# Kernel tuning notes

Hardware: AMD Instinct MI355X
Metric: run time of the kernel (lower is better)

The kernel has to match this reference:

```python
import jax, jax.numpy as jnp
import numpy as np

N = 4096   # support size
B = 512    # number of histograms (columns)


def setup_inputs() -> dict:
    key = jax.random.key(0)
    kU, kP, kK = jax.random.split(key, 3)
    # u must satisfy u < lamda; uniform [0,1) with lamda=10 is safe.
    U = jax.random.uniform(kU, (N, B), dtype=jnp.float32)
    # strictly positive histograms (avoid log(0))
    P = jax.random.uniform(kP, (N, B), dtype=jnp.float32) + 0.01
    # positive Gibbs kernel
    K = jax.random.uniform(kK, (N, N), dtype=jnp.float32) + 1e-3
    return {"U": U, "P": P, "K": K, "eps": 1, "lamda": 10}


def reference(U, P, K, eps, lamda):
    """Vectorized OTModel.OT_unbal: sum over columns of the primal unbalanced OT
    value reconstructed from dual potential U.  gamma_ij = a_i * K_ij * f_j is
    never materialized; all reductions over gamma are contracted analytically.
    """
    eps = jnp.float32(eps)
    lamda = jnp.float32(lamda)
    # f in log domain: (lamda/eps) * log(lamda/(lamda-u))          [N, B]
    flog = (lamda / eps) * jnp.log(lamda / (lamda - U))
    f = jnp.exp(flog)
    # alpha/eps with the mean-scale stabilization from get_alpha_unbal
    scale = flog.mean(axis=0)                                      # [B]
    KF_stab = K @ jnp.exp(flog - scale)                            # [N, B]
    alpha_over_eps = jnp.log(P) - (jnp.log(KF_stab) + scale)       # [N, B]
    a = jnp.exp(alpha_over_eps)                                    # exp(alpha/eps)
    Kf = K @ f                                                     # [N, B]
    # (gamma @ flog).sum() = sum_i a_i * (K @ (f * flog))_i
    term1 = jnp.sum(a * (K @ (f * flog)))
    # (gamma.T @ (alpha/eps)).sum() = sum_i a_i * (alpha/eps)_i * (K @ f)_i
    term2 = jnp.sum(a * alpha_over_eps * Kf)
    # gamma.sum()
    term3 = jnp.sum(a * Kf)
    # gamma.sum(0)_j = f_j * (K^T @ a)_j
    gcol = f * (K.T @ a)                                           # [N, B]
    # q from get_q_unbal (unstabilized, as in the original)
    q = (lamda / (lamda - U)) ** (lamda / eps + 1.0) * (K.T @ (P / Kf))
    # KL(a,b) = sum(a*log(a/b) - a)   (inputs strictly positive here)
    kl = jnp.sum(gcol * jnp.log(gcol / q) - gcol)
    return eps * (term1 + term2 - term3) + lamda * kl
```

## Files before the change

### kernel.cpp

```cpp
#include <hip/hip_runtime.h>

#define NN 4096
#define BB 512

typedef __attribute__((ext_vector_type(4))) float f32x4;
typedef __attribute__((ext_vector_type(2))) long long2v;
typedef unsigned short ushort;
typedef unsigned char uchar;
typedef unsigned int uint;
typedef __attribute__((ext_vector_type(4))) ushort ushort4v;

#define ASCALE 16384.0f
#define AINV   6.103515625e-05f

__device__ __forceinline__ float scal_val(const void* p) {
    int b = *(const int*)p;
    if (b >= 1 && b <= 1000000) return (float)b;
    return __int_as_float(b);
}

__device__ __forceinline__ ushort f2bf(float x) {
    unsigned u = __float_as_uint(x);
    u += 0x7fffu + ((u >> 16) & 1u);
    return (ushort)(u >> 16);
}
__device__ __forceinline__ float bf2f(ushort b) {
    return __uint_as_float((uint)b << 16);
}

__device__ __forceinline__ uint pack4_fp8(float a, float b, float c, float d) {
    int v = __builtin_amdgcn_cvt_pk_fp8_f32(a, b, 0, false);
    v = __builtin_amdgcn_cvt_pk_fp8_f32(c, d, v, true);
    return (uint)v;
}

__device__ __forceinline__ void gload16(const void* g, void* l) {
    __builtin_amdgcn_global_load_lds(
        (const __attribute__((address_space(1))) unsigned int*)g,
        (__attribute__((address_space(3))) unsigned int*)l, 16, 0, 0);
}

__device__ __forceinline__ double wave_sum(double v) {
#pragma unroll
    for (int s = 32; s > 0; s >>= 1) v += __shfl_down(v, s, 64);
    return v;
}

__device__ __forceinline__ int kperm(int kk) {
    int c = kk >> 3;
    return (c & 3) * 16 + (c >> 2) * 8 + (kk & 7);
}
__device__ __forceinline__ int bpos(int row, int pp) {
    return (((pp >> 4) ^ ((row >> 1) & 3)) << 4) | (pp & 15);
}



__global__ __launch_bounds__(256) void k_prep(const float* __restrict__ K,
                                              const float* __restrict__ U,
                                              uchar* __restrict__ Kb,
                                              uchar* __restrict__ KTb,
                                              uchar* __restrict__ fT,
                                              const void* epsp, const void* lamp) {
    __shared__ float tile[64][65];
    const int t = threadIdx.x;
    const int tx = t & 15, ty = t >> 4;
    const int bid = blockIdx.x;
    const int pp = kperm(tx * 4);

    if (bid < 4096) {
        const int c0 = (bid & 63) * 64, r0 = (bid >> 6) * 64;
#pragma unroll
        for (int it = 0; it < 4; ++it) {
            int row = ty + it * 16;
            float4 v = *(const float4*)&K[(size_t)(r0 + row) * NN + c0 + tx * 4];
            int i = r0 + row;
            int off = (((i >> 7) * 64 + (c0 >> 6)) << 13) + (i & 127) * 64 +
                      bpos(row, pp);
            *(uint*)&Kb[off] = pack4_fp8(v.x, v.y, v.z, v.w);
            tile[row][tx * 4 + 0] = v.x;
            tile[row][tx * 4 + 1] = v.y;
            tile[row][tx * 4 + 2] = v.z;
            tile[row][tx * 4 + 3] = v.w;
        }
        __syncthreads();
#pragma unroll
        for (int it = 0; it < 4; ++it) {
            int row = ty + it * 16;
            int i = c0 + row;
            int off = (((i >> 7) * 64 + (r0 >> 6)) << 13) + (i & 127) * 64 +
                      bpos(row, pp);
            *(uint*)&KTb[off] =
                pack4_fp8(tile[tx * 4 + 0][row], tile[tx * 4 + 1][row],
                          tile[tx * 4 + 2][row], tile[tx * 4 + 3][row]);
        }
    } else {
        const int r = bid - 4096;
        const int c0 = (r & 7) * 64;
        const int r0 = (r >> 3) * 64;
        const float eps = scal_val(epsp), lam = scal_val(lamp);
        const float rr = lam / eps;
#pragma unroll
        for (int it = 0; it < 4; ++it) {
            int row = ty + it * 16;
            float4 v = *(const float4*)&U[(size_t)(r0 + row) * BB + c0 + tx * 4];
            float uu[4] = {v.x, v.y, v.z, v.w};
#pragma unroll
            for (int k = 0; k < 4; ++k) {
                float L = __logf(lam / (lam - uu[k]));
                tile[row][tx * 4 + k] = __expf(rr * L);
            }
        }
        __syncthreads();
#pragma unroll
        for (int it = 0; it < 4; ++it) {
            int row = ty + it * 16;
            int j = c0 + row;
            int off = (((j >> 6) * 64 + (r0 >> 6)) << 12) + (j & 63) * 64 +
                      bpos(row, pp);
            *(uint*)&fT[off] =
                pack4_fp8(tile[tx * 4 + 0][row], tile[tx * 4 + 1][row],
                          tile[tx * 4 + 2][row], tile[tx * 4 + 3][row]);
        }
    }
}

__global__ __launch_bounds__(256) void k_gemm1(const uchar* __restrict__ Kb,
                                               const uchar* __restrict__ fT,
                                               ushort* __restrict__ Y1b) {
    __shared__ __align__(16) uchar As[2][128 * 64];
    __shared__ __align__(16) uchar Bf[2][64 * 64];

    const int tid = threadIdx.x;
    const int lane = tid & 63;
    const int w = tid >> 6;
    const int wm = w & 1, wn = w >> 1;
    const int bid = blockIdx.x;
    const int kh = bid & 3;
    const int i0 = ((bid >> 2) & 31) * 128;
    const int j0 = (bid >> 7) * 64;
    const int quad = lane >> 4;
    const int l15 = lane & 15;
    const int sw = (l15 >> 1) & 3;

    f32x4 zero = {0.f, 0.f, 0.f, 0.f};
    f32x4 acc[4][2];
#pragma unroll
    for (int mt = 0; mt < 4; ++mt)
#pragma unroll
        for (int nt = 0; nt < 2; ++nt) acc[mt][nt] = zero;

    const uchar* apanel = Kb + ((size_t)(i0 >> 7) << 19);
    const uchar* bpanel = fT + ((size_t)(j0 >> 6) << 18);

    auto stage = [&](int ks, int b) {
        const uchar* ga = apanel + ((size_t)ks << 13) + w * 2048 + lane * 16;
        gload16(ga, &As[b][w * 2048]);
        gload16(ga + 1024, &As[b][w * 2048 + 1024]);
        const uchar* gb = bpanel + ((size_t)ks << 12) + w * 1024 + lane * 16;
        gload16(gb, &Bf[b][w * 1024]);
    };

    const int ks0 = kh * 16;
    stage(ks0, 0);
    __syncthreads();
    const int uoff = ((quad ^ sw) << 4);
    for (int step = 0; step < 16; ++step) {
        const int cur = step & 1;
        if (step < 15) stage(ks0 + step + 1, cur ^ 1);
        long2v av[4], bv[2];
#pragma unroll
        for (int mt = 0; mt < 4; ++mt)
            av[mt] = *(const long2v*)&As[cur][(wm * 64 + mt * 16 + l15) * 64 + uoff];
#pragma unroll
        for (int nt = 0; nt < 2; ++nt)
            bv[nt] = *(const long2v*)&Bf[cur][(wn * 32 + nt * 16 + l15) * 64 + uoff];
#pragma unroll
        for (int mt = 0; mt < 4; ++mt)
#pragma unroll
            for (int nt = 0; nt < 2; ++nt) {
                acc[mt][nt] = __builtin_amdgcn_mfma_f32_16x16x32_fp8_fp8(
                    av[mt].x, bv[nt].x, acc[mt][nt], 0, 0, 0);
                acc[mt][nt] = __builtin_amdgcn_mfma_f32_16x16x32_fp8_fp8(
                    av[mt].y, bv[nt].y, acc[mt][nt], 0, 0, 0);
            }
        __syncthreads();
    }

    ushort* o1 = Y1b + (size_t)kh * NN * BB;
#pragma unroll
    for (int mt = 0; mt < 4; ++mt)
#pragma unroll
        for (int nt = 0; nt < 2; ++nt) {
            const int ib = i0 + wm * 64 + mt * 16 + quad * 4;
            const int j = j0 + wn * 32 + nt * 16 + l15;
#pragma unroll
            for (int r = 0; r < 4; ++r)
                o1[(size_t)(ib + r) * BB + j] = f2bf(acc[mt][nt][r]);
        }
}

__global__ __launch_bounds__(256) void k_epi(const ushort* __restrict__ Y1b,
                                             const float* __restrict__ P,
                                             uchar* __restrict__ aT,
                                             double* __restrict__ parts) {
    __shared__ float ta[64][65];
    __shared__ double bred[4][2];
    const int t = threadIdx.x;
    const int lane = t & 63;
    const int w = t >> 6;
    const int tx = t & 15, ty = t >> 4;
    const int j0 = blockIdx.x * 64;
    const int i0 = blockIdx.y * 64;
    const int bid = blockIdx.y * 8 + blockIdx.x;
    const size_t H = (size_t)NN * BB;
    const int pp = kperm(tx * 4);

    double t2 = 0.0, t3 = 0.0;
#pragma unroll
    for (int it = 0; it < 4; ++it) {
        int row = ty + it * 16;
        size_t off = (size_t)(i0 + row) * BB + j0 + tx * 4;
        ushort4v q0 = *(const ushort4v*)(Y1b + off);
        ushort4v q1 = *(const ushort4v*)(Y1b + H + off);
        ushort4v q2 = *(const ushort4v*)(Y1b + 2 * H + off);
        ushort4v q3 = *(const ushort4v*)(Y1b + 3 * H + off);
        float4 p4 = *(const float4*)(P + off);
        float pv[4] = {p4.x, p4.y, p4.z, p4.w};
#pragma unroll
        for (int e = 0; e < 4; ++e) {
            float y1 = bf2f(q0[e]) + bf2f(q1[e]) + bf2f(q2[e]) + bf2f(q3[e]);
            float aij = pv[e] / y1;
            t2 += (double)(pv[e] * __logf(aij));
            t3 += (double)pv[e];
            ta[row][tx * 4 + e] = aij * ASCALE;
        }
    }
    __syncthreads();
#pragma unroll
    for (int it = 0; it < 4; ++it) {
        int row = ty + it * 16;
        int j = j0 + row;
        int off = (((j >> 6) * 64 + (i0 >> 6)) << 12) + (j & 63) * 64 +
                  bpos(row, pp);
        *(uint*)&aT[off] =
            pack4_fp8(ta[tx * 4 + 0][row], ta[tx * 4 + 1][row],
                      ta[tx * 4 + 2][row], ta[tx * 4 + 3][row]);
    }

    t2 = wave_sum(t2); t3 = wave_sum(t3);
    if (lane == 0) { bred[w][0] = t2; bred[w][1] = t3; }
    __syncthreads();
    if (t == 0) {
        double b = 0, c = 0;
#pragma unroll
        for (int ww = 0; ww < 4; ++ww) { b += bred[ww][0]; c += bred[ww][1]; }
        parts[2048 + bid] = b;
        parts[2560 + bid] = c;
    }
}

__global__ __launch_bounds__(256) void k_gemm2(const uchar* __restrict__ KTb,
                                               const uchar* __restrict__ aT,
                                               const float* __restrict__ U,
                                               const void* epsp, const void* lamp,
                                               double* __restrict__ parts) {
    __shared__ __align__(16) uchar As[2][128 * 64];
    __shared__ __align__(16) uchar Bs[2][64 * 64];
    __shared__ double bred[4][2];

    const float eps = scal_val(epsp), lam = scal_val(lamp);
    const float rr = lam / eps;
    const int tid = threadIdx.x;
    const int lane = tid & 63;
    const int w = tid >> 6;
    const int wm = w & 1, wn = w >> 1;
    const int bid = blockIdx.x;
    const int kh = bid & 3;
    const int i0 = ((bid >> 2) & 31) * 128;
    const int j0 = (bid >> 7) * 64;
    const int quad = lane >> 4;
    const int l15 = lane & 15;
    const int sw = (l15 >> 1) & 3;

    f32x4 zero = {0.f, 0.f, 0.f, 0.f};
    f32x4 acc[4][2];
#pragma unroll
    for (int mt = 0; mt < 4; ++mt)
#pragma unroll
        for (int nt = 0; nt < 2; ++nt) acc[mt][nt] = zero;

    const uchar* apanel = KTb + ((size_t)(i0 >> 7) << 19);
    const uchar* bpanel = aT + ((size_t)(j0 >> 6) << 18);

    auto stage = [&](int ks, int b) {
        const uchar* ga = apanel + ((size_t)ks << 13) + w * 2048 + lane * 16;
        gload16(ga, &As[b][w * 2048]);
        gload16(ga + 1024, &As[b][w * 2048 + 1024]);
        const uchar* gb = bpanel + ((size_t)ks << 12) + w * 1024 + lane * 16;
        gload16(gb, &Bs[b][w * 1024]);
    };

    const int ks0 = kh * 16;
    stage(ks0, 0);
    __syncthreads();
    const int uoff = ((quad ^ sw) << 4);
    for (int step = 0; step < 16; ++step) {
        const int cur = step & 1;
        if (step < 15) stage(ks0 + step + 1, cur ^ 1);
        long2v av[4], bv[2];
#pragma unroll
        for (int mt = 0; mt < 4; ++mt)
            av[mt] = *(const long2v*)&As[cur][(wm * 64 + mt * 16 + l15) * 64 + uoff];
#pragma unroll
        for (int nt = 0; nt < 2; ++nt)
            bv[nt] = *(const long2v*)&Bs[cur][(wn * 32 + nt * 16 + l15) * 64 + uoff];
#pragma unroll
        for (int mt = 0; mt < 4; ++mt)
#pragma unroll
            for (int nt = 0; nt < 2; ++nt) {
                acc[mt][nt] = __builtin_amdgcn_mfma_f32_16x16x32_fp8_fp8(
                    av[mt].x, bv[nt].x, acc[mt][nt], 0, 0, 0);
                acc[mt][nt] = __builtin_amdgcn_mfma_f32_16x16x32_fp8_fp8(
                    av[mt].y, bv[nt].y, acc[mt][nt], 0, 0, 0);
            }
        __syncthreads();
    }

    double t1p = 0.0, klp = 0.0;
#pragma unroll
    for (int mt = 0; mt < 4; ++mt)
#pragma unroll
        for (int nt = 0; nt < 2; ++nt) {
            const int ib = i0 + wm * 64 + mt * 16 + quad * 4;
            const int j = j0 + wn * 32 + nt * 16 + l15;
#pragma unroll
            for (int r = 0; r < 4; ++r) {
                float s = acc[mt][nt][r] * AINV;
                float u = U[(size_t)(ib + r) * BB + j];
                float L = __logf(lam / (lam - u));
                float fv = __expf(rr * L);
                t1p += (double)(fv * rr * L * s);
                klp -= (double)(fv * (1.0f + L) * s);
            }
        }

    t1p = wave_sum(t1p); klp = wave_sum(klp);
    if (lane == 0) { bred[w][0] = t1p; bred[w][1] = klp; }
    __syncthreads();
    if (tid == 0) {
        double a = 0, b = 0;
#pragma unroll
        for (int ww = 0; ww < 4; ++ww) { a += bred[ww][0]; b += bred[ww][1]; }
        parts[bid] = a;
        parts[1024 + bid] = b;
    }
}

__global__ __launch_bounds__(256) void k_final(const double* __restrict__ parts,
                                               const void* epsp, const void* lamp,
                                               float* __restrict__ out) {
    __shared__ double red[4][4];
    const int tid = threadIdx.x;
    const int lane = tid & 63, w = tid >> 6;
    double s0 = 0.0, s1 = 0.0, s2 = 0.0, s3 = 0.0;
    for (int i = tid; i < 1024; i += 256) {
        s0 += parts[i];
        s1 += parts[1024 + i];
    }
    for (int i = tid; i < 512; i += 256) {
        s2 += parts[2048 + i];
        s3 += parts[2560 + i];
    }
    s0 = wave_sum(s0); s1 = wave_sum(s1); s2 = wave_sum(s2); s3 = wave_sum(s3);
    if (lane == 0) { red[w][0] = s0; red[w][1] = s1; red[w][2] = s2; red[w][3] = s3; }
    __syncthreads();
    if (tid == 0) {
        double t1 = 0, kl = 0, t2 = 0, t3 = 0;
#pragma unroll
        for (int ww = 0; ww < 4; ++ww) {
            t1 += red[ww][0]; kl += red[ww][1]; t2 += red[ww][2]; t3 += red[ww][3];
        }
        float eps = scal_val(epsp), lam = scal_val(lamp);
        out[0] = (float)((double)eps * (t1 + t2 - t3) + (double)lam * kl);
    }
}

extern "C" void kernel_launch(void* const* d_in, const int* in_sizes, int n_in,
                              void* d_out, int out_size, void* d_ws, size_t ws_size,
                              hipStream_t stream) {
    const float* U = (const float*)d_in[0];
    const float* P = (const float*)d_in[1];
    const float* K = (const float*)d_in[2];
    const void* epsp = d_in[3];
    const void* lamp = d_in[4];

    double* parts = (double*)d_ws;
    char* base = (char*)d_ws + (64 << 10);
    uchar* Kb   = (uchar*)base;
    uchar* KTb  = (uchar*)(base + ((size_t)16 << 20));
    uchar* fT   = (uchar*)(base + ((size_t)32 << 20));
    uchar* aT   = (uchar*)(base + ((size_t)34 << 20));
    ushort* Y1b = (ushort*)(base + ((size_t)36 << 20));

    k_prep<<<4608, 256, 0, stream>>>(K, U, Kb, KTb, fT, epsp, lamp);
    k_gemm1<<<1024, 256, 0, stream>>>(Kb, fT, Y1b);
    k_epi<<<dim3(8, 64), 256, 0, stream>>>(Y1b, P, aT, parts);
    k_gemm2<<<1024, 256, 0, stream>>>(KTb, aT, U, epsp, lamp, parts);
    k_final<<<1, 256, 0, stream>>>(parts, epsp, lamp, (float*)d_out);
}
```

Before: 164.6 us.

## Switch FP8 GEMMs to 16x16x128 scaled MFMA with 128-wide K tiles

Both GEMMs now use the gfx950 scaled MFMA 16x16x128 f8f6f4 instruction with unit scales in place of pairs of 16x16x32 fp8 MFMAs. The packed fp8 layouts for K, K^T, f and a are rewritten into 128-byte K rows with an XOR swizzle, and the LDS tiles double in size. Split-K drops from 4 to 2, which halves the grid to 512 blocks, and the partial sums are stored as fp32 instead of bf16 so the epilogue reads two slabs instead of four. The change cuts the MFMA instruction count and split-K reduction traffic, at the cost of fewer blocks in flight and more LDS per block, which may lower occupancy.

```diff
diff --git a/kernel.cpp b/kernel.cpp
--- a/kernel.cpp
+++ b/kernel.cpp
@@ -4,14 +4,15 @@
 #define BB 512
 
 typedef __attribute__((ext_vector_type(4))) float f32x4;
-typedef __attribute__((ext_vector_type(2))) long long2v;
+typedef __attribute__((ext_vector_type(4))) int i32x4;
+typedef __attribute__((ext_vector_type(8))) int i32x8;
 typedef unsigned short ushort;
 typedef unsigned char uchar;
 typedef unsigned int uint;
-typedef __attribute__((ext_vector_type(4))) ushort ushort4v;
 
 #define ASCALE 16384.0f
 #define AINV   6.103515625e-05f
+#define SCL1   0x7f7f7f7f
 
 __device__ __forceinline__ float scal_val(const void* p) {
     int b = *(const int*)p;
@@ -19,15 +20,6 @@
     return __int_as_float(b);
 }
 
-__device__ __forceinline__ ushort f2bf(float x) {
-    unsigned u = __float_as_uint(x);
-    u += 0x7fffu + ((u >> 16) & 1u);
-    return (ushort)(u >> 16);
-}
-__device__ __forceinline__ float bf2f(ushort b) {
-    return __uint_as_float((uint)b << 16);
-}
-
 __device__ __forceinline__ uint pack4_fp8(float a, float b, float c, float d) {
     int v = __builtin_amdgcn_cvt_pk_fp8_f32(a, b, 0, false);
     v = __builtin_amdgcn_cvt_pk_fp8_f32(c, d, v, true);
@@ -46,14 +38,23 @@
     return v;
 }
 
-__device__ __forceinline__ int kperm(int kk) {
-    int c = kk >> 3;
-    return (c & 3) * 16 + (c >> 2) * 8 + (kk & 7);
-}
-__device__ __forceinline__ int bpos(int row, int pp) {
-    return (((pp >> 4) ^ ((row >> 1) & 3)) << 4) | (pp & 15);
-}
-
+__device__ __forceinline__ int offA(int i, int k) {
+    return (((i >> 7) * 32 + (k >> 7)) << 14) + ((i & 127) << 7) +
+           ((((k >> 4) & 7) ^ (i & 7)) << 4) + (k & 15);
+}
+__device__ __forceinline__ int offB(int j, int k) {
+    return (((j >> 6) * 32 + (k >> 7)) << 13) + ((j & 63) << 7) +
+           ((((k >> 4) & 7) ^ (j & 7)) << 4) + (k & 15);
+}
+
+__device__ __forceinline__ i32x8 frag128(const uchar* rowbase, int u0byte) {
+    i32x4 lo = *(const i32x4*)(rowbase + u0byte);
+    i32x4 hi = *(const i32x4*)(rowbase + (u0byte ^ 16));
+    i32x8 r;
+    r[0] = lo[0]; r[1] = lo[1]; r[2] = lo[2]; r[3] = lo[3];
+    r[4] = hi[0]; r[5] = hi[1]; r[6] = hi[2]; r[7] = hi[3];
+    return r;
+}
 
 
 __global__ __launch_bounds__(256) void k_prep(const float* __restrict__ K,
@@ -66,18 +67,15 @@
     const int t = threadIdx.x;
     const int tx = t & 15, ty = t >> 4;
     const int bid = blockIdx.x;
-    const int pp = kperm(tx * 4);
 
     if (bid < 4096) {
         const int c0 = (bid & 63) * 64, r0 = (bid >> 6) * 64;
 #pragma unroll
         for (int it = 0; it < 4; ++it) {
             int row = ty + it * 16;
-            float4 v = *(const float4*)&K[(size_t)(r0 + row) * NN + c0 + tx * 4];
             int i = r0 + row;
-            int off = (((i >> 7) * 64 + (c0 >> 6)) << 13) + (i & 127) * 64 +
-                      bpos(row, pp);
-            *(uint*)&Kb[off] = pack4_fp8(v.x, v.y, v.z, v.w);
+            float4 v = *(const float4*)&K[(size_t)i * NN + c0 + tx * 4];
+            *(uint*)&Kb[offA(i, c0 + tx * 4)] = pack4_fp8(v.x, v.y, v.z, v.w);
             tile[row][tx * 4 + 0] = v.x;
             tile[row][tx * 4 + 1] = v.y;
             tile[row][tx * 4 + 2] = v.z;
@@ -88,9 +86,8 @@
         for (int it = 0; it < 4; ++it) {
             int row = ty + it * 16;
             int i = c0 + row;
-            int off = (((i >> 7) * 64 + (r0 >> 6)) << 13) + (i & 127) * 64 +
-                      bpos(row, pp);
-            *(uint*)&KTb[off] =
+            int k = r0 + tx * 4;
+            *(uint*)&KTb[offA(i, k)] =
                 pack4_fp8(tile[tx * 4 + 0][row], tile[tx * 4 + 1][row],
                           tile[tx * 4 + 2][row], tile[tx * 4 + 3][row]);
         }
@@ -116,9 +113,8 @@
         for (int it = 0; it < 4; ++it) {
             int row = ty + it * 16;
             int j = c0 + row;
-            int off = (((j >> 6) * 64 + (r0 >> 6)) << 12) + (j & 63) * 64 +
-                      bpos(row, pp);
-            *(uint*)&fT[off] =
+            int k = r0 + tx * 4;
+            *(uint*)&fT[offB(j, k)] =
                 pack4_fp8(tile[tx * 4 + 0][row], tile[tx * 4 + 1][row],
                           tile[tx * 4 + 2][row], tile[tx * 4 + 3][row]);
         }
@@ -127,21 +123,21 @@
 
 __global__ __launch_bounds__(256) void k_gemm1(const uchar* __restrict__ Kb,
                                                const uchar* __restrict__ fT,
-                                               ushort* __restrict__ Y1b) {
-    __shared__ __align__(16) uchar As[2][128 * 64];
-    __shared__ __align__(16) uchar Bf[2][64 * 64];
+                                               float* __restrict__ Y1f) {
+    __shared__ __align__(16) uchar As[2][128 * 128];
+    __shared__ __align__(16) uchar Bf[2][64 * 128];
 
     const int tid = threadIdx.x;
     const int lane = tid & 63;
     const int w = tid >> 6;
     const int wm = w & 1, wn = w >> 1;
     const int bid = blockIdx.x;
-    const int kh = bid & 3;
-    const int i0 = ((bid >> 2) & 31) * 128;
-    const int j0 = (bid >> 7) * 64;
+    const int kh = bid & 1;
+    const int i0 = ((bid >> 1) & 31) * 128;
+    const int j0 = (bid >> 6) * 64;
     const int quad = lane >> 4;
     const int l15 = lane & 15;
-    const int sw = (l15 >> 1) & 3;
+    const int u0b = (((quad << 1) ^ (l15 & 7)) << 4);
 
     f32x4 zero = {0.f, 0.f, 0.f, 0.f};
     f32x4 acc[4][2];
@@ -154,40 +150,39 @@
     const uchar* bpanel = fT + ((size_t)(j0 >> 6) << 18);
 
     auto stage = [&](int ks, int b) {
-        const uchar* ga = apanel + ((size_t)ks << 13) + w * 2048 + lane * 16;
-        gload16(ga, &As[b][w * 2048]);
-        gload16(ga + 1024, &As[b][w * 2048 + 1024]);
-        const uchar* gb = bpanel + ((size_t)ks << 12) + w * 1024 + lane * 16;
-        gload16(gb, &Bf[b][w * 1024]);
+        const uchar* ga = apanel + ((size_t)ks << 14) + w * 4096 + lane * 16;
+        gload16(ga, &As[b][w * 4096]);
+        gload16(ga + 1024, &As[b][w * 4096 + 1024]);
+        gload16(ga + 2048, &As[b][w * 4096 + 2048]);
+        gload16(ga + 3072, &As[b][w * 4096 + 3072]);
+        const uchar* gb = bpanel + ((size_t)ks << 13) + w * 2048 + lane * 16;
+        gload16(gb, &Bf[b][w * 2048]);
+        gload16(gb + 1024, &Bf[b][w * 2048 + 1024]);
     };
 
     const int ks0 = kh * 16;
     stage(ks0, 0);
     __syncthreads();
-    const int uoff = ((quad ^ sw) << 4);
     for (int step = 0; step < 16; ++step) {
         const int cur = step & 1;
         if (step < 15) stage(ks0 + step + 1, cur ^ 1);
-        long2v av[4], bv[2];
+        i32x8 av[4], bv[2];
 #pragma unroll
         for (int mt = 0; mt < 4; ++mt)
-            av[mt] = *(const long2v*)&As[cur][(wm * 64 + mt * 16 + l15) * 64 + uoff];
+            av[mt] = frag128(&As[cur][(wm * 64 + mt * 16 + l15) << 7], u0b);
 #pragma unroll
         for (int nt = 0; nt < 2; ++nt)
-            bv[nt] = *(const long2v*)&Bf[cur][(wn * 32 + nt * 16 + l15) * 64 + uoff];
+            bv[nt] = frag128(&Bf[cur][(wn * 32 + nt * 16 + l15) << 7], u0b);
 #pragma unroll
         for (int mt = 0; mt < 4; ++mt)
 #pragma unroll
-            for (int nt = 0; nt < 2; ++nt) {
-                acc[mt][nt] = __builtin_amdgcn_mfma_f32_16x16x32_fp8_fp8(
-                    av[mt].x, bv[nt].x, acc[mt][nt], 0, 0, 0);
-                acc[mt][nt] = __builtin_amdgcn_mfma_f32_16x16x32_fp8_fp8(
-                    av[mt].y, bv[nt].y, acc[mt][nt], 0, 0, 0);
-            }
+            for (int nt = 0; nt < 2; ++nt)
+                acc[mt][nt] = __builtin_amdgcn_mfma_scale_f32_16x16x128_f8f6f4(
+                    av[mt], bv[nt], acc[mt][nt], 0, 0, 0, SCL1, 0, SCL1);
         __syncthreads();
     }
 
-    ushort* o1 = Y1b + (size_t)kh * NN * BB;
+    float* o1 = Y1f + (size_t)kh * NN * BB;
 #pragma unroll
     for (int mt = 0; mt < 4; ++mt)
 #pragma unroll
@@ -196,11 +191,11 @@
             const int j = j0 + wn * 32 + nt * 16 + l15;
 #pragma unroll
             for (int r = 0; r < 4; ++r)
-                o1[(size_t)(ib + r) * BB + j] = f2bf(acc[mt][nt][r]);
-        }
-}
-
-__global__ __launch_bounds__(256) void k_epi(const ushort* __restrict__ Y1b,
+                o1[(size_t)(ib + r) * BB + j] = acc[mt][nt][r];
+        }
+}
+
+__global__ __launch_bounds__(256) void k_epi(const float* __restrict__ Y1f,
                                              const float* __restrict__ P,
                                              uchar* __restrict__ aT,
                                              double* __restrict__ parts) {
@@ -214,25 +209,21 @@
     const int i0 = blockIdx.y * 64;
     const int bid = blockIdx.y * 8 + blockIdx.x;
     const size_t H = (size_t)NN * BB;
-    const int pp = kperm(tx * 4);
 
     double t2 = 0.0, t3 = 0.0;
 #pragma unroll
     for (int it = 0; it < 4; ++it) {
         int row = ty + it * 16;
         size_t off = (size_t)(i0 + row) * BB + j0 + tx * 4;
-        ushort4v q0 = *(const ushort4v*)(Y1b + off);
-        ushort4v q1 = *(const ushort4v*)(Y1b + H + off);
-        ushort4v q2 = *(const ushort4v*)(Y1b + 2 * H + off);
-        ushort4v q3 = *(const ushort4v*)(Y1b + 3 * H + off);
-        float4 p4 = *(const float4*)(P + off);
-        float pv[4] = {p4.x, p4.y, p4.z, p4.w};
+        f32x4 q0 = *(const f32x4*)(Y1f + off);
+        f32x4 q1 = *(const f32x4*)(Y1f + H + off);
+        f32x4 p4 = *(const f32x4*)(P + off);
 #pragma unroll
         for (int e = 0; e < 4; ++e) {
-            float y1 = bf2f(q0[e]) + bf2f(q1[e]) + bf2f(q2[e]) + bf2f(q3[e]);
-            float aij = pv[e] / y1;
-            t2 += (double)(pv[e] * __logf(aij));
-            t3 += (double)pv[e];
+            float y1 = q0[e] + q1[e];
+            float aij = p4[e] / y1;
+            t2 += (double)(p4[e] * __logf(aij));
+            t3 += (double)p4[e];
             ta[row][tx * 4 + e] = aij * ASCALE;
         }
     }
@@ -241,9 +232,7 @@
     for (int it = 0; it < 4; ++it) {
         int row = ty + it * 16;
         int j = j0 + row;
-        int off = (((j >> 6) * 64 + (i0 >> 6)) << 12) + (j & 63) * 64 +
-                  bpos(row, pp);
-        *(uint*)&aT[off] =
+        *(uint*)&aT[offB(j, i0 + tx * 4)] =
             pack4_fp8(ta[tx * 4 + 0][row], ta[tx * 4 + 1][row],
                       ta[tx * 4 + 2][row], ta[tx * 4 + 3][row]);
     }
@@ -265,8 +254,8 @@
                                                const float* __restrict__ U,
                                                const void* epsp, const void* lamp,
                                                double* __restrict__ parts) {
-    __shared__ __align__(16) uchar As[2][128 * 64];
-    __shared__ __align__(16) uchar Bs[2][64 * 64];
+    __shared__ __align__(16) uchar As[2][128 * 128];
+    __shared__ __align__(16) uchar Bs[2][64 * 128];
     __shared__ double bred[4][2];
 
     const float eps = scal_val(epsp), lam = scal_val(lamp);
@@ -276,12 +265,12 @@
     const int w = tid >> 6;
     const int wm = w & 1, wn = w >> 1;
     const int bid = blockIdx.x;
-    const int kh = bid & 3;
-    const int i0 = ((bid >> 2) & 31) * 128;
-    const int j0 = (bid >> 7) * 64;
+    const int kh = bid & 1;
+    const int i0 = ((bid >> 1) & 31) * 128;
+    const int j0 = (bid >> 6) * 64;
     const int quad = lane >> 4;
     const int l15 = lane & 15;
-    const int sw = (l15 >> 1) & 3;
+    const int u0b = (((quad << 1) ^ (l15 & 7)) << 4);
 
     f32x4 zero = {0.f, 0.f, 0.f, 0.f};
     f32x4 acc[4][2];
@@ -294,36 +283,35 @@
     const uchar* bpanel = aT + ((size_t)(j0 >> 6) << 18);
 
     auto stage = [&](int ks, int b) {
-        const uchar* ga = apanel + ((size_t)ks << 13) + w * 2048 + lane * 16;
-        gload16(ga, &As[b][w * 2048]);
-        gload16(ga + 1024, &As[b][w * 2048 + 1024]);
-        const uchar* gb = bpanel + ((size_t)ks << 12) + w * 1024 + lane * 16;
-        gload16(gb, &Bs[b][w * 1024]);
+        const uchar* ga = apanel + ((size_t)ks << 14) + w * 4096 + lane * 16;
+        gload16(ga, &As[b][w * 4096]);
+        gload16(ga + 1024, &As[b][w * 4096 + 1024]);
+        gload16(ga + 2048, &As[b][w * 4096 + 2048]);
+        gload16(ga + 3072, &As[b][w * 4096 + 3072]);
+        const uchar* gb = bpanel + ((size_t)ks << 13) + w * 2048 + lane * 16;
+        gload16(gb, &Bs[b][w * 2048]);
+        gload16(gb + 1024, &Bs[b][w * 2048 + 1024]);
     };
 
     const int ks0 = kh * 16;
     stage(ks0, 0);
     __syncthreads();
-    const int uoff = ((quad ^ sw) << 4);
     for (int step = 0; step < 16; ++step) {
         const int cur = step & 1;
         if (step < 15) stage(ks0 + step + 1, cur ^ 1);
-        long2v av[4], bv[2];
+        i32x8 av[4], bv[2];
 #pragma unroll
         for (int mt = 0; mt < 4; ++mt)
-            av[mt] = *(const long2v*)&As[cur][(wm * 64 + mt * 16 + l15) * 64 + uoff];
+            av[mt] = frag128(&As[cur][(wm * 64 + mt * 16 + l15) << 7], u0b);
 #pragma unroll
         for (int nt = 0; nt < 2; ++nt)
-            bv[nt] = *(const long2v*)&Bs[cur][(wn * 32 + nt * 16 + l15) * 64 + uoff];
+            bv[nt] = frag128(&Bs[cur][(wn * 32 + nt * 16 + l15) << 7], u0b);
 #pragma unroll
         for (int mt = 0; mt < 4; ++mt)
 #pragma unroll
-            for (int nt = 0; nt < 2; ++nt) {
-                acc[mt][nt] = __builtin_amdgcn_mfma_f32_16x16x32_fp8_fp8(
-                    av[mt].x, bv[nt].x, acc[mt][nt], 0, 0, 0);
-                acc[mt][nt] = __builtin_amdgcn_mfma_f32_16x16x32_fp8_fp8(
-                    av[mt].y, bv[nt].y, acc[mt][nt], 0, 0, 0);
-            }
+            for (int nt = 0; nt < 2; ++nt)
+                acc[mt][nt] = __builtin_amdgcn_mfma_scale_f32_16x16x128_f8f6f4(
+                    av[mt], bv[nt], acc[mt][nt], 0, 0, 0, SCL1, 0, SCL1);
         __syncthreads();
     }
 
@@ -364,11 +352,9 @@
     const int tid = threadIdx.x;
     const int lane = tid & 63, w = tid >> 6;
     double s0 = 0.0, s1 = 0.0, s2 = 0.0, s3 = 0.0;
-    for (int i = tid; i < 1024; i += 256) {
+    for (int i = tid; i < 512; i += 256) {
         s0 += parts[i];
         s1 += parts[1024 + i];
-    }
-    for (int i = tid; i < 512; i += 256) {
         s2 += parts[2048 + i];
         s3 += parts[2560 + i];
     }
@@ -401,11 +387,11 @@
     uchar* KTb  = (uchar*)(base + ((size_t)16 << 20));
     uchar* fT   = (uchar*)(base + ((size_t)32 << 20));
     uchar* aT   = (uchar*)(base + ((size_t)34 << 20));
-    ushort* Y1b = (ushort*)(base + ((size_t)36 << 20));
+    float* Y1f  = (float*)(base + ((size_t)36 << 20));
 
     k_prep<<<4608, 256, 0, stream>>>(K, U, Kb, KTb, fT, epsp, lamp);
-    k_gemm1<<<1024, 256, 0, stream>>>(Kb, fT, Y1b);
-    k_epi<<<dim3(8, 64), 256, 0, stream>>>(Y1b, P, aT, parts);
-    k_gemm2<<<1024, 256, 0, stream>>>(KTb, aT, U, epsp, lamp, parts);
+    k_gemm1<<<512, 256, 0, stream>>>(Kb, fT, Y1f);
+    k_epi<<<dim3(8, 64), 256, 0, stream>>>(Y1f, P, aT, parts);
+    k_gemm2<<<512, 256, 0, stream>>>(KTb, aT, U, epsp, lamp, parts);
     k_final<<<1, 256, 0, stream>>>(parts, epsp, lamp, (float*)d_out);
 }
```

After: 167.9 us. Within noise of the previous version (+2.0%).

## Switch FP8 GEMMs to 32x32x64 scaled MFMA with a new swizzled layout

Applied to the files above, without the earlier changes.

Both FP8 GEMM kernels now issue the MI355X scaled MFMA (32x32x64 f8f6f4, unit scales) instead of many 16x16x32 fp8 MFMAs. Each wave owns a 32-row strip and the full 64 columns, so it makes two large MFMAs per k-step and fewer LDS fragment reads. The prep and epilogue kernels write K, K^T, f^T and a^T with a new swizzle that matches the 64-byte fragments. The wave-to-tile mapping changes, so B fragments are read by every wave and the epilogue store and reduction indexing change too.

```diff
diff --git a/kernel.cpp b/kernel.cpp
--- a/kernel.cpp
+++ b/kernel.cpp
@@ -4,7 +4,9 @@
 #define BB 512
 
 typedef __attribute__((ext_vector_type(4))) float f32x4;
-typedef __attribute__((ext_vector_type(2))) long long2v;
+typedef __attribute__((ext_vector_type(16))) float f32x16;
+typedef __attribute__((ext_vector_type(4))) int i32x4;
+typedef __attribute__((ext_vector_type(8))) int i32x8;
 typedef unsigned short ushort;
 typedef unsigned char uchar;
 typedef unsigned int uint;
@@ -12,6 +14,7 @@
 
 #define ASCALE 16384.0f
 #define AINV   6.103515625e-05f
+#define SCL1   0x7f7f7f7f
 
 __device__ __forceinline__ float scal_val(const void* p) {
     int b = *(const int*)p;
@@ -46,14 +49,23 @@
     return v;
 }
 
-__device__ __forceinline__ int kperm(int kk) {
-    int c = kk >> 3;
-    return (c & 3) * 16 + (c >> 2) * 8 + (kk & 7);
-}
-__device__ __forceinline__ int bpos(int row, int pp) {
-    return (((pp >> 4) ^ ((row >> 1) & 3)) << 4) | (pp & 15);
-}
-
+__device__ __forceinline__ int offA(int i, int k) {
+    return (((i >> 7) * 64 + (k >> 6)) << 13) + ((i & 127) << 6) +
+           ((((k >> 4) & 3) ^ ((i >> 1) & 3)) << 4) + (k & 15);
+}
+__device__ __forceinline__ int offB(int j, int k) {
+    return (((j >> 6) * 64 + (k >> 6)) << 12) + ((j & 63) << 6) +
+           ((((k >> 4) & 3) ^ ((j >> 1) & 3)) << 4) + (k & 15);
+}
+
+__device__ __forceinline__ i32x8 frag64(const uchar* rowbase, int u0byte) {
+    i32x4 lo = *(const i32x4*)(rowbase + u0byte);
+    i32x4 hi = *(const i32x4*)(rowbase + (u0byte ^ 16));
+    i32x8 r;
+    r[0] = lo[0]; r[1] = lo[1]; r[2] = lo[2]; r[3] = lo[3];
+    r[4] = hi[0]; r[5] = hi[1]; r[6] = hi[2]; r[7] = hi[3];
+    return r;
+}
 
 
 __global__ __launch_bounds__(256) void k_prep(const float* __restrict__ K,
@@ -66,18 +78,15 @@
     const int t = threadIdx.x;
     const int tx = t & 15, ty = t >> 4;
     const int bid = blockIdx.x;
-    const int pp = kperm(tx * 4);
 
     if (bid < 4096) {
         const int c0 = (bid & 63) * 64, r0 = (bid >> 6) * 64;
 #pragma unroll
         for (int it = 0; it < 4; ++it) {
             int row = ty + it * 16;
-            float4 v = *(const float4*)&K[(size_t)(r0 + row) * NN + c0 + tx * 4];
             int i = r0 + row;
-            int off = (((i >> 7) * 64 + (c0 >> 6)) << 13) + (i & 127) * 64 +
-                      bpos(row, pp);
-            *(uint*)&Kb[off] = pack4_fp8(v.x, v.y, v.z, v.w);
+            float4 v = *(const float4*)&K[(size_t)i * NN + c0 + tx * 4];
+            *(uint*)&Kb[offA(i, c0 + tx * 4)] = pack4_fp8(v.x, v.y, v.z, v.w);
             tile[row][tx * 4 + 0] = v.x;
             tile[row][tx * 4 + 1] = v.y;
             tile[row][tx * 4 + 2] = v.z;
@@ -88,9 +97,8 @@
         for (int it = 0; it < 4; ++it) {
             int row = ty + it * 16;
             int i = c0 + row;
-            int off = (((i >> 7) * 64 + (r0 >> 6)) << 13) + (i & 127) * 64 +
-                      bpos(row, pp);
-            *(uint*)&KTb[off] =
+            int k = r0 + tx * 4;
+            *(uint*)&KTb[offA(i, k)] =
                 pack4_fp8(tile[tx * 4 + 0][row], tile[tx * 4 + 1][row],
                           tile[tx * 4 + 2][row], tile[tx * 4 + 3][row]);
         }
@@ -116,9 +124,8 @@
         for (int it = 0; it < 4; ++it) {
             int row = ty + it * 16;
             int j = c0 + row;
-            int off = (((j >> 6) * 64 + (r0 >> 6)) << 12) + (j & 63) * 64 +
-                      bpos(row, pp);
-            *(uint*)&fT[off] =
+            int k = r0 + tx * 4;
+            *(uint*)&fT[offB(j, k)] =
                 pack4_fp8(tile[tx * 4 + 0][row], tile[tx * 4 + 1][row],
                           tile[tx * 4 + 2][row], tile[tx * 4 + 3][row]);
         }
@@ -134,21 +141,15 @@
     const int tid = threadIdx.x;
     const int lane = tid & 63;
     const int w = tid >> 6;
-    const int wm = w & 1, wn = w >> 1;
     const int bid = blockIdx.x;
     const int kh = bid & 3;
     const int i0 = ((bid >> 2) & 31) * 128;
     const int j0 = (bid >> 7) * 64;
-    const int quad = lane >> 4;
-    const int l15 = lane & 15;
-    const int sw = (l15 >> 1) & 3;
-
-    f32x4 zero = {0.f, 0.f, 0.f, 0.f};
-    f32x4 acc[4][2];
-#pragma unroll
-    for (int mt = 0; mt < 4; ++mt)
-#pragma unroll
-        for (int nt = 0; nt < 2; ++nt) acc[mt][nt] = zero;
+    const int h = lane >> 5;
+    const int r = lane & 31;
+    const int u0b = (((h << 1) ^ ((r >> 1) & 3)) << 4);
+
+    f32x16 acc0 = {}, acc1 = {};
 
     const uchar* apanel = Kb + ((size_t)(i0 >> 7) << 19);
     const uchar* bpanel = fT + ((size_t)(j0 >> 6) << 18);
@@ -164,40 +165,26 @@
     const int ks0 = kh * 16;
     stage(ks0, 0);
     __syncthreads();
-    const int uoff = ((quad ^ sw) << 4);
     for (int step = 0; step < 16; ++step) {
         const int cur = step & 1;
         if (step < 15) stage(ks0 + step + 1, cur ^ 1);
-        long2v av[4], bv[2];
-#pragma unroll
-        for (int mt = 0; mt < 4; ++mt)
-            av[mt] = *(const long2v*)&As[cur][(wm * 64 + mt * 16 + l15) * 64 + uoff];
-#pragma unroll
-        for (int nt = 0; nt < 2; ++nt)
-            bv[nt] = *(const long2v*)&Bf[cur][(wn * 32 + nt * 16 + l15) * 64 + uoff];
-#pragma unroll
-        for (int mt = 0; mt < 4; ++mt)
-#pragma unroll
-            for (int nt = 0; nt < 2; ++nt) {
-                acc[mt][nt] = __builtin_amdgcn_mfma_f32_16x16x32_fp8_fp8(
-                    av[mt].x, bv[nt].x, acc[mt][nt], 0, 0, 0);
-                acc[mt][nt] = __builtin_amdgcn_mfma_f32_16x16x32_fp8_fp8(
-                    av[mt].y, bv[nt].y, acc[mt][nt], 0, 0, 0);
-            }
+        i32x8 av = frag64(&As[cur][(w * 32 + r) << 6], u0b);
+        i32x8 bv0 = frag64(&Bf[cur][r << 6], u0b);
+        i32x8 bv1 = frag64(&Bf[cur][(32 + r) << 6], u0b);
+        acc0 = __builtin_amdgcn_mfma_scale_f32_32x32x64_f8f6f4(
+            av, bv0, acc0, 0, 0, 0, SCL1, 0, SCL1);
+        acc1 = __builtin_amdgcn_mfma_scale_f32_32x32x64_f8f6f4(
+            av, bv1, acc1, 0, 0, 0, SCL1, 0, SCL1);
         __syncthreads();
     }
 
     ushort* o1 = Y1b + (size_t)kh * NN * BB;
 #pragma unroll
-    for (int mt = 0; mt < 4; ++mt)
-#pragma unroll
-        for (int nt = 0; nt < 2; ++nt) {
-            const int ib = i0 + wm * 64 + mt * 16 + quad * 4;
-            const int j = j0 + wn * 32 + nt * 16 + l15;
-#pragma unroll
-            for (int r = 0; r < 4; ++r)
-                o1[(size_t)(ib + r) * BB + j] = f2bf(acc[mt][nt][r]);
-        }
+    for (int reg = 0; reg < 16; ++reg) {
+        const int row = i0 + w * 32 + (reg & 3) + 8 * (reg >> 2) + 4 * h;
+        o1[(size_t)row * BB + j0 + r] = f2bf(acc0[reg]);
+        o1[(size_t)row * BB + j0 + 32 + r] = f2bf(acc1[reg]);
+    }
 }
 
 __global__ __launch_bounds__(256) void k_epi(const ushort* __restrict__ Y1b,
@@ -214,7 +201,6 @@
     const int i0 = blockIdx.y * 64;
     const int bid = blockIdx.y * 8 + blockIdx.x;
     const size_t H = (size_t)NN * BB;
-    const int pp = kperm(tx * 4);
 
     double t2 = 0.0, t3 = 0.0;
 #pragma unroll
@@ -241,9 +227,7 @@
     for (int it = 0; it < 4; ++it) {
         int row = ty + it * 16;
         int j = j0 + row;
-        int off = (((j >> 6) * 64 + (i0 >> 6)) << 12) + (j & 63) * 64 +
-                  bpos(row, pp);
-        *(uint*)&aT[off] =
+        *(uint*)&aT[offB(j, i0 + tx * 4)] =
             pack4_fp8(ta[tx * 4 + 0][row], ta[tx * 4 + 1][row],
                       ta[tx * 4 + 2][row], ta[tx * 4 + 3][row]);
     }
@@ -274,21 +258,15 @@
     const int tid = threadIdx.x;
     const int lane = tid & 63;
     const int w = tid >> 6;
-    const int wm = w & 1, wn = w >> 1;
     const int bid = blockIdx.x;
     const int kh = bid & 3;
     const int i0 = ((bid >> 2) & 31) * 128;
     const int j0 = (bid >> 7) * 64;
-    const int quad = lane >> 4;
-    const int l15 = lane & 15;
-    const int sw = (l15 >> 1) & 3;
-
-    f32x4 zero = {0.f, 0.f, 0.f, 0.f};
-    f32x4 acc[4][2];
-#pragma unroll
-    for (int mt = 0; mt < 4; ++mt)
-#pragma unroll
-        for (int nt = 0; nt < 2; ++nt) acc[mt][nt] = zero;
+    const int h = lane >> 5;
+    const int r = lane & 31;
+    const int u0b = (((h << 1) ^ ((r >> 1) & 3)) << 4);
+
+    f32x16 acc0 = {}, acc1 = {};
 
     const uchar* apanel = KTb + ((size_t)(i0 >> 7) << 19);
     const uchar* bpanel = aT + ((size_t)(j0 >> 6) << 18);
@@ -304,46 +282,34 @@
     const int ks0 = kh * 16;
     stage(ks0, 0);
     __syncthreads();
-    const int uoff = ((quad ^ sw) << 4);
     for (int step = 0; step < 16; ++step) {
         const int cur = step & 1;
         if (step < 15) stage(ks0 + step + 1, cur ^ 1);
-        long2v av[4], bv[2];
-#pragma unroll
-        for (int mt = 0; mt < 4; ++mt)
-            av[mt] = *(const long2v*)&As[cur][(wm * 64 + mt * 16 + l15) * 64 + uoff];
-#pragma unroll
-        for (int nt = 0; nt < 2; ++nt)
-            bv[nt] = *(const long2v*)&Bs[cur][(wn * 32 + nt * 16 + l15) * 64 + uoff];
-#pragma unroll
-        for (int mt = 0; mt < 4; ++mt)
-#pragma unroll
-            for (int nt = 0; nt < 2; ++nt) {
-                acc[mt][nt] = __builtin_amdgcn_mfma_f32_16x16x32_fp8_fp8(
-                    av[mt].x, bv[nt].x, acc[mt][nt], 0, 0, 0);
-                acc[mt][nt] = __builtin_amdgcn_mfma_f32_16x16x32_fp8_fp8(
-                    av[mt].y, bv[nt].y, acc[mt][nt], 0, 0, 0);
-            }
+        i32x8 av = frag64(&As[cur][(w * 32 + r) << 6], u0b);
+        i32x8 bv0 = frag64(&Bs[cur][r << 6], u0b);
+        i32x8 bv1 = frag64(&Bs[cur][(32 + r) << 6], u0b);
+        acc0 = __builtin_amdgcn_mfma_scale_f32_32x32x64_f8f6f4(
+            av, bv0, acc0, 0, 0, 0, SCL1, 0, SCL1);
+        acc1 = __builtin_amdgcn_mfma_scale_f32_32x32x64_f8f6f4(
+            av, bv1, acc1, 0, 0, 0, SCL1, 0, SCL1);
         __syncthreads();
     }
 
     double t1p = 0.0, klp = 0.0;
 #pragma unroll
-    for (int mt = 0; mt < 4; ++mt)
+    for (int reg = 0; reg < 16; ++reg) {
+        const int ib = i0 + w * 32 + (reg & 3) + 8 * (reg >> 2) + 4 * h;
 #pragma unroll
         for (int nt = 0; nt < 2; ++nt) {
-            const int ib = i0 + wm * 64 + mt * 16 + quad * 4;
-            const int j = j0 + wn * 32 + nt * 16 + l15;
-#pragma unroll
-            for (int r = 0; r < 4; ++r) {
-                float s = acc[mt][nt][r] * AINV;
-                float u = U[(size_t)(ib + r) * BB + j];
-                float L = __logf(lam / (lam - u));
-                float fv = __expf(rr * L);
-                t1p += (double)(fv * rr * L * s);
-                klp -= (double)(fv * (1.0f + L) * s);
-            }
-        }
+            const int j = j0 + nt * 32 + r;
+            float s = (nt ? acc1[reg] : acc0[reg]) * AINV;
+            float u = U[(size_t)ib * BB + j];
+            float L = __logf(lam / (lam - u));
+            float fv = __expf(rr * L);
+            t1p += (double)(fv * rr * L * s);
+            klp -= (double)(fv * (1.0f + L) * s);
+        }
+    }
 
     t1p = wave_sum(t1p); klp = wave_sum(klp);
     if (lane == 0) { bred[w][0] = t1p; bred[w][1] = klp; }
```

Measured after the change: 156.0 us. 1.06x faster.
